# Kernel optimization log

Measured on AMD Instinct MI355X. Metric: run time of the kernel, lower is better.

Reference implementation:

```python
import jax, jax.numpy as jnp
import numpy as np
import math

INPUT_SIZE = 256
HIDDEN_SIZE = 1024
TIMESTEPS = 32768


def setup_inputs() -> dict:
    key = jax.random.key(0)
    ks = jax.random.split(key, 7)
    stdv = 1.0 / math.sqrt(HIDDEN_SIZE)
    u = lambda k, shape: jax.random.uniform(k, shape, jnp.float32, -stdv, stdv)
    return {
        "input_data": jax.random.normal(ks[0], (TIMESTEPS, 1, INPUT_SIZE), jnp.float32),
        "weight_ih": u(ks[1], (HIDDEN_SIZE, INPUT_SIZE)),
        "weight_hh": u(ks[2], (HIDDEN_SIZE, HIDDEN_SIZE)),
        "weight": u(ks[3], (HIDDEN_SIZE,)),
        "bias_ih": u(ks[4], (HIDDEN_SIZE,)),
        "bias_hh": u(ks[5], (HIDDEN_SIZE,)),
        "bias": u(ks[6], (HIDDEN_SIZE,)),
    }


def reference(input_data, weight_ih, weight_hh, weight, bias_ih, bias_hh, bias):
    # input_data: [T, 1, F] (batch must be 1, as in the original flatten-based matmuls)
    T, B, F = input_data.shape
    x = input_data.reshape(T, F)
    # Precompute all input projections as one GEMM: [T, H]
    xW = x @ weight_ih.T

    def step(h, xw):
        hW = weight_hh @ h  # [H]
        h_new = jnp.tanh(weight * xw * hW + bias_ih * xw + bias_hh * hW + bias)
        return h_new, h_new

    h0 = jnp.zeros((weight_hh.shape[0],), dtype=input_data.dtype)
    _, ys = jax.lax.scan(step, h0, xW)
    return ys[:, None, :]  # [T, 1, H]
```

## Files before the change

kernel.cpp:

```cpp
#include <hip/hip_runtime.h>
#include <hip/hip_bf16.h>
#include <stdint.h>

#define T_STEPS 32768
#define HID 1024
#define FIN 256
#define NB_SCAN 32
#define NB_HEAT 8
#define RPB 32
#define RPW 8
#define WORDS (HID / 2)

typedef unsigned long long ull;

__global__ __launch_bounds__(256) void gemm_xw(const float* __restrict__ x,
                                               const float* __restrict__ wih,
                                               float* __restrict__ out) {
    __shared__ float As[32][132];
    __shared__ float Bs[32][132];
    const int tid = threadIdx.x;
    const int m0 = blockIdx.y * 128;
    const int n0 = blockIdx.x * 128;
    const int tm = tid >> 4, tn = tid & 15;
    const int lr = tid >> 1, lc = (tid & 1) * 16;

    float acc[8][8];
#pragma unroll
    for (int i = 0; i < 8; ++i)
#pragma unroll
        for (int j = 0; j < 8; ++j) acc[i][j] = 0.f;

    for (int kk = 0; kk < FIN; kk += 32) {
#pragma unroll
        for (int u = 0; u < 4; ++u) {
            float4 av = *reinterpret_cast<const float4*>(
                &x[(size_t)(m0 + lr) * FIN + kk + lc + 4 * u]);
            float4 bv = *reinterpret_cast<const float4*>(
                &wih[(size_t)(n0 + lr) * FIN + kk + lc + 4 * u]);
            As[lc + 4 * u + 0][lr] = av.x;
            As[lc + 4 * u + 1][lr] = av.y;
            As[lc + 4 * u + 2][lr] = av.z;
            As[lc + 4 * u + 3][lr] = av.w;
            Bs[lc + 4 * u + 0][lr] = bv.x;
            Bs[lc + 4 * u + 1][lr] = bv.y;
            Bs[lc + 4 * u + 2][lr] = bv.z;
            Bs[lc + 4 * u + 3][lr] = bv.w;
        }
        __syncthreads();
#pragma unroll
        for (int k = 0; k < 32; ++k) {
            const float4* Ak = reinterpret_cast<const float4*>(&As[k][0]);
            const float4* Bk = reinterpret_cast<const float4*>(&Bs[k][0]);
            float4 a0 = Ak[tm * 2], a1 = Ak[tm * 2 + 1];
            float4 b0 = Bk[tn * 2], b1 = Bk[tn * 2 + 1];
            float a[8] = {a0.x, a0.y, a0.z, a0.w, a1.x, a1.y, a1.z, a1.w};
            float b[8] = {b0.x, b0.y, b0.z, b0.w, b1.x, b1.y, b1.z, b1.w};
#pragma unroll
            for (int i = 0; i < 8; ++i)
#pragma unroll
                for (int j = 0; j < 8; ++j) acc[i][j] = fmaf(a[i], b[j], acc[i][j]);
        }
        __syncthreads();
    }
#pragma unroll
    for (int i = 0; i < 8; ++i) {
        float4 o0 = make_float4(acc[i][0], acc[i][1], acc[i][2], acc[i][3]);
        float4 o1 = make_float4(acc[i][4], acc[i][5], acc[i][6], acc[i][7]);
        float* op = &out[(size_t)(m0 + tm * 8 + i) * HID + n0 + tn * 8];
        *reinterpret_cast<float4*>(op) = o0;
        *reinterpret_cast<float4*>(op + 4) = o1;
    }
}

__device__ __forceinline__ float fast_tanh(float x) {
    float cx = fminf(fmaxf(x, -16.f), 16.f);
    float e = __builtin_amdgcn_exp2f(cx * 2.8853900817779268f);
    return (e - 1.f) * __builtin_amdgcn_rcpf(e + 1.f);
}

__device__ __forceinline__ void barrier_lds_only() {
    asm volatile("s_waitcnt lgkmcnt(0)\n\ts_barrier" ::: "memory");
}

__device__ __forceinline__ void poll8(const ull* __restrict__ src, int lane,
                                      ull (&v)[8]) {
#pragma unroll
    for (int i = 0; i < 8; ++i)
        v[i] = __hip_atomic_load(src + lane + 64 * i, __ATOMIC_RELAXED,
                                 __HIP_MEMORY_SCOPE_AGENT);
}

__device__ __forceinline__ bool check8(const ull (&v)[8], unsigned expb) {
    unsigned d = 0;
#pragma unroll
    for (int i = 0; i < 8; ++i) d |= (((unsigned)v[i]) ^ expb) & 0xFFu;
    return d == 0;
}

__device__ void heater_body(const int* quit, const float* __restrict__ mem,
                            int bi, int tid) {
    float a0 = tid * 0.001f + 1.f, a1 = a0 + 1.f, a2 = a0 + 2.f, a3 = a0 + 3.f;
    float a4 = a0 + 4.f, a5 = a0 + 5.f, a6 = a0 + 6.f, a7 = a0 + 7.f;
    size_t idx = ((size_t)bi * 256 + tid) * 4;
    const size_t mask = (32u * 1024u * 1024u) - 1u;
    for (int it = 0; it < 400000; ++it) {
        float4 v = *reinterpret_cast<const float4*>(&mem[idx & mask & ~3ull]);
        a0 = fmaf(v.x, 1e-30f, a0);
#pragma unroll 64
        for (int u = 0; u < 64; ++u) {
            a0 = fmaf(a0, 1.0000001f, 0.5f);
            a1 = fmaf(a1, 1.0000001f, 0.5f);
            a2 = fmaf(a2, 1.0000001f, 0.5f);
            a3 = fmaf(a3, 1.0000001f, 0.5f);
            a4 = fmaf(a4, 1.0000001f, 0.5f);
            a5 = fmaf(a5, 1.0000001f, 0.5f);
            a6 = fmaf(a6, 1.0000001f, 0.5f);
            a7 = fmaf(a7, 1.0000001f, 0.5f);
        }
        idx += 64 * 2048;
        if (__hip_atomic_load(quit, __ATOMIC_RELAXED, __HIP_MEMORY_SCOPE_AGENT))
            break;
    }
    asm volatile("" ::"v"(a0), "v"(a1), "v"(a2), "v"(a3), "v"(a4), "v"(a5),
                 "v"(a6), "v"(a7));
}

__global__ __launch_bounds__(256, 1) void scan_rnn(
    const float* __restrict__ whh, const float* __restrict__ wgt,
    const float* __restrict__ bih, const float* __restrict__ bhh,
    const float* __restrict__ bb, float* __restrict__ out,
    ull* __restrict__ hbuf, int* __restrict__ quit) {
    if (blockIdx.x >= NB_SCAN) {
        heater_body(quit, out, blockIdx.x - NB_SCAN, threadIdx.x);
        return;
    }
    __shared__ ull hshw[WORDS];
    const int lane = threadIdx.x & 63;
    const int wv = threadIdx.x >> 6;
    const int r0 = blockIdx.x * RPB + wv * RPW;
    const int rr = r0 + (lane & 7);

    float wreg[RPW][16];
#pragma unroll
    for (int j = 0; j < RPW; ++j)
#pragma unroll
        for (int i = 0; i < 16; ++i)
            wreg[j][i] = whh[(size_t)(r0 + j) * HID + lane + 64 * i];

    const float cw = wgt[rr], cbi = bih[rr], cbh = bhh[rr], cb = bb[rr];
    float xw_cur = out[rr];

    for (int t = 0; t < T_STEPS; ++t) {
        if (wv == 0) {
            const ull* src = hbuf + (size_t)(t & 1) * WORDS;
            const unsigned expb = (unsigned)t & 0xFFu;
            ull va[8], vb[8];
            poll8(src, lane, va);
            for (;;) {
                poll8(src, lane, vb);
                if (check8(va, expb)) {
#pragma unroll
                    for (int i = 0; i < 8; ++i) hshw[lane + 64 * i] = va[i];
                    break;
                }
                poll8(src, lane, va);
                if (check8(vb, expb)) {
#pragma unroll
                    for (int i = 0; i < 8; ++i) hshw[lane + 64 * i] = vb[i];
                    break;
                }
                __builtin_amdgcn_s_sleep(1);
            }
        }
        barrier_lds_only();

        const float* hf = (const float*)(&hshw[0]);
        float hval[16];
#pragma unroll
        for (int i = 0; i < 16; ++i) hval[i] = hf[lane + 64 * i];

        float acc[RPW];
#pragma unroll
        for (int j = 0; j < RPW; ++j) acc[j] = 0.f;
#pragma unroll
        for (int i = 0; i < 16; ++i)
#pragma unroll
            for (int j = 0; j < RPW; ++j)
                acc[j] = fmaf(wreg[j][i], hval[i], acc[j]);

#pragma unroll
        for (int m = 1; m < 8; m <<= 1)
#pragma unroll
            for (int j = 0; j < RPW; ++j) acc[j] += __shfl_xor(acc[j], m, 64);
        float y = acc[0];
#pragma unroll
        for (int j = 1; j < RPW; ++j) y = ((lane & 7) == j) ? acc[j] : y;
#pragma unroll
        for (int m = 8; m < 64; m <<= 1) y += __shfl_xor(y, m, 64);

        const float arg = fmaf(fmaf(cw, xw_cur, cbh), y, fmaf(cbi, xw_cur, cb));
        const float hn = fast_tanh(arg);
        const float hnp = __shfl_xor(hn, 1, 64);

        if (lane < 8) {
            if ((lane & 1) == 0) {
                unsigned lo = (__float_as_uint(hn) & 0xFFFFFF00u) |
                              ((unsigned)(t + 1) & 0xFFu);
                ull pv = ((ull)__float_as_uint(hnp) << 32) | (ull)lo;
                __hip_atomic_store(
                    hbuf + (size_t)((t + 1) & 1) * WORDS + (r0 >> 1) +
                        (lane >> 1),
                    pv, __ATOMIC_RELAXED, __HIP_MEMORY_SCOPE_AGENT);
            }
            out[(size_t)t * HID + rr] = hn;
        }
        const int nt = t < T_STEPS - 1 ? t + 1 : t;
        xw_cur = out[(size_t)nt * HID + rr];
    }
    if (blockIdx.x == 0 && threadIdx.x == 0)
        __hip_atomic_store(quit, 1, __ATOMIC_RELAXED, __HIP_MEMORY_SCOPE_AGENT);
}

extern "C" void kernel_launch(void* const* d_in, const int* in_sizes, int n_in,
                              void* d_out, int out_size, void* d_ws, size_t ws_size,
                              hipStream_t stream) {
    const float* x = (const float*)d_in[0];
    const float* wih = (const float*)d_in[1];
    const float* whh = (const float*)d_in[2];
    const float* wgt = (const float*)d_in[3];
    const float* bih = (const float*)d_in[4];
    const float* bhh = (const float*)d_in[5];
    const float* bb = (const float*)d_in[6];
    float* out = (float*)d_out;

    ull* hbuf = (ull*)d_ws;
    int* quit = (int*)((char*)d_ws + 2 * WORDS * sizeof(ull));
    hipMemsetAsync(d_ws, 0, 2 * WORDS * sizeof(ull) + 128, stream);

    dim3 ggrid(HID / 128, T_STEPS / 128);
    gemm_xw<<<ggrid, 256, 0, stream>>>(x, wih, out);

    scan_rnn<<<NB_SCAN + NB_HEAT, 256, 0, stream>>>(whh, wgt, bih, bhh, bb,
                                                    out, hbuf, quit);
}
```

Before: 69.22 ms.

## Poll hidden-state flags with 16-byte inline-asm loads and more heater blocks

Replaces the per-lane 8-byte relaxed atomic polls of the shared hidden-state buffer with inline-assembly dwordx4 loads using sc0/sc1 cache bypass. Two poll batches are kept in flight with explicit vmcnt waits, and a fallback to the old poll loop triggers after repeated misses. Each 32-bit half of the packed word now carries its own step tag so a 16-byte read can be validated per dword. This costs extra mantissa truncation on the high half. The heater block count also rises from 8 to 64, which adds memory pressure that may slow the scan blocks.

After: 79.82 ms. 15.3% more time.

```diff
diff --git a/kernel.cpp b/kernel.cpp
--- a/kernel.cpp
+++ b/kernel.cpp
@@ -6,7 +6,7 @@
 #define HID 1024
 #define FIN 256
 #define NB_SCAN 32
-#define NB_HEAT 8
+#define NB_HEAT 64
 #define RPB 32
 #define RPW 8
 #define WORDS (HID / 2)
@@ -80,6 +80,29 @@
 
 __device__ __forceinline__ void barrier_lds_only() {
     asm volatile("s_waitcnt lgkmcnt(0)\n\ts_barrier" ::: "memory");
+}
+
+__device__ __forceinline__ void pollx4_issue(const char* base, uint4 (&v)[4]) {
+    asm volatile(
+        "global_load_dwordx4 %0, %[a], off sc0 sc1\n\t"
+        "global_load_dwordx4 %1, %[a], off offset:1024 sc0 sc1\n\t"
+        "global_load_dwordx4 %2, %[a], off offset:2048 sc0 sc1\n\t"
+        "global_load_dwordx4 %3, %[a], off offset:3072 sc0 sc1"
+        : "=&v"(v[0]), "=&v"(v[1]), "=&v"(v[2]), "=&v"(v[3])
+        : [a] "v"(base)
+        : "memory");
+}
+
+__device__ __forceinline__ bool checkx4(const uint4 (&v)[4], unsigned expb) {
+    unsigned d = 0;
+#pragma unroll
+    for (int i = 0; i < 4; ++i) {
+        d |= (v[i].x ^ expb) & 0xFFu;
+        d |= (v[i].y ^ expb) & 0xFFu;
+        d |= (v[i].z ^ expb) & 0xFFu;
+        d |= (v[i].w ^ expb) & 0xFFu;
+    }
+    return d == 0;
 }
 
 __device__ __forceinline__ void poll8(const ull* __restrict__ src, int lane,
@@ -134,7 +157,7 @@
         heater_body(quit, out, blockIdx.x - NB_SCAN, threadIdx.x);
         return;
     }
-    __shared__ ull hshw[WORDS];
+    __shared__ __align__(16) ull hshw[WORDS];
     const int lane = threadIdx.x & 63;
     const int wv = threadIdx.x >> 6;
     const int r0 = blockIdx.x * RPB + wv * RPW;
@@ -149,27 +172,68 @@
 
     const float cw = wgt[rr], cbi = bih[rr], cbh = bhh[rr], cb = bb[rr];
     float xw_cur = out[rr];
+    bool asm_ok = true;
+    uint32_t* hsh32 = (uint32_t*)hshw;
 
     for (int t = 0; t < T_STEPS; ++t) {
         if (wv == 0) {
             const ull* src = hbuf + (size_t)(t & 1) * WORDS;
             const unsigned expb = (unsigned)t & 0xFFu;
-            ull va[8], vb[8];
-            poll8(src, lane, va);
-            for (;;) {
-                poll8(src, lane, vb);
-                if (check8(va, expb)) {
-#pragma unroll
-                    for (int i = 0; i < 8; ++i) hshw[lane + 64 * i] = va[i];
-                    break;
+            bool hit = false;
+            if (asm_ok) {
+                const char* base = (const char*)src + lane * 16;
+                uint4 va[4], vb[4];
+                asm volatile("s_waitcnt vmcnt(0)" ::: "memory");
+                pollx4_issue(base, va);
+                pollx4_issue(base, vb);
+                int miss = 0;
+                for (;;) {
+                    asm volatile("s_waitcnt vmcnt(4)" ::: "memory");
+                    if (checkx4(va, expb)) {
+#pragma unroll
+                        for (int i = 0; i < 4; ++i)
+                            *(uint4*)&hsh32[4 * (lane + 64 * i)] = va[i];
+                        hit = true;
+                        break;
+                    }
+                    pollx4_issue(base, va);
+                    asm volatile("s_waitcnt vmcnt(4)" ::: "memory");
+                    if (checkx4(vb, expb)) {
+#pragma unroll
+                        for (int i = 0; i < 4; ++i)
+                            *(uint4*)&hsh32[4 * (lane + 64 * i)] = vb[i];
+                        hit = true;
+                        break;
+                    }
+                    pollx4_issue(base, vb);
+                    if (++miss > 32) {
+                        asm_ok = false;
+                        asm volatile("s_waitcnt vmcnt(0)" ::: "memory");
+                        break;
+                    }
+                    __builtin_amdgcn_s_sleep(1);
                 }
+            }
+            if (!hit) {
+                ull va[8], vb[8];
                 poll8(src, lane, va);
-                if (check8(vb, expb)) {
-#pragma unroll
-                    for (int i = 0; i < 8; ++i) hshw[lane + 64 * i] = vb[i];
-                    break;
+                for (;;) {
+                    poll8(src, lane, vb);
+                    if (check8(va, expb)) {
+#pragma unroll
+                        for (int i = 0; i < 8; ++i)
+                            hshw[lane + 64 * i] = va[i];
+                        break;
+                    }
+                    poll8(src, lane, va);
+                    if (check8(vb, expb)) {
+#pragma unroll
+                        for (int i = 0; i < 8; ++i)
+                            hshw[lane + 64 * i] = vb[i];
+                        break;
+                    }
+                    __builtin_amdgcn_s_sleep(1);
                 }
-                __builtin_amdgcn_s_sleep(1);
             }
         }
         barrier_lds_only();
@@ -204,9 +268,10 @@
 
         if (lane < 8) {
             if ((lane & 1) == 0) {
-                unsigned lo = (__float_as_uint(hn) & 0xFFFFFF00u) |
-                              ((unsigned)(t + 1) & 0xFFu);
-                ull pv = ((ull)__float_as_uint(hnp) << 32) | (ull)lo;
+                const unsigned tagb = (unsigned)(t + 1) & 0xFFu;
+                unsigned lo = (__float_as_uint(hn) & 0xFFFFFF00u) | tagb;
+                unsigned hi = (__float_as_uint(hnp) & 0xFFFFFF00u) | tagb;
+                ull pv = ((ull)hi << 32) | (ull)lo;
                 __hip_atomic_store(
                     hbuf + (size_t)((t + 1) & 1) * WORDS + (r0 >> 1) +
                         (lane >> 1),
```
